# Optimization experiments

Hardware: AMD Instinct MI355X
Metric: run time of the kernel (lower is better)

Reference implementation:

```python
import jax, jax.numpy as jnp
import numpy as np

EPS = 1e-8


def setup_inputs() -> dict:
    key = jax.random.key(0)
    ks = jax.random.split(key, 11)
    N, D_OBS, D_AC, K = 2_000_000, 32, 16, 128
    H = int(1.66 * K)  # 212, matches int(1.66*k) in the torch module
    s = 0.05
    return {
        "obs": jax.random.normal(ks[0], (N, D_OBS), dtype=jnp.float32),
        "acs": jax.random.normal(ks[1], (N, D_AC), dtype=jnp.float32),
        "x": jax.random.normal(ks[2], (D_OBS,), dtype=jnp.float32),
        "w_in": jax.random.normal(ks[3], (H, K), dtype=jnp.float32) * s,
        "b_in": jax.random.normal(ks[4], (H,), dtype=jnp.float32) * s,
        "w2": jax.random.normal(ks[5], (H, H), dtype=jnp.float32) * s,
        "b2": jax.random.normal(ks[6], (H,), dtype=jnp.float32) * s,
        "w3": jax.random.normal(ks[7], (H, H), dtype=jnp.float32) * s,
        "b3": jax.random.normal(ks[8], (H,), dtype=jnp.float32) * s,
        "w_out": jax.random.normal(ks[9], (K, H), dtype=jnp.float32) * s,
        "b_out": jax.random.normal(ks[10], (K,), dtype=jnp.float32) * s,
        "k": K,
    }


def reference(obs, acs, x, w_in, b_in, w2, b2, w3, b3, w_out, b_out, k):
    # cosine distance between every obs row and the query x: [N]
    xn = x * jax.lax.rsqrt(jnp.sum(x * x) + EPS)
    obs_nrm = jax.lax.rsqrt(jnp.sum(obs * obs, axis=1) + EPS)  # [N]
    cos_sim = (obs @ xn) * obs_nrm                              # [N]
    cos_dist = 1.0 - cos_sim                                    # [N]

    # top-k smallest distances (argpartition equivalent, sorted ascending)
    neg_vals, idx = jax.lax.top_k(-cos_dist, k)                 # [k], [k]
    k_cos_dist = -neg_vals                                      # [k]
    k_actions = acs[idx]                                        # [k, D_ac]

    # tiny MLP on the k distances -> softmax weights over the k neighbors
    h = jax.nn.relu(k_cos_dist @ w_in.T + b_in)
    h = jax.nn.relu(h @ w2.T + b2)
    h = jax.nn.relu(h @ w3.T + b3)
    weights = jax.nn.softmax(h @ w_out.T + b_out)               # [k]

    # weighted sum of the k neighbor actions -> [1, D_ac]
    out = jnp.sum(weights[:, None] * k_actions, axis=0, keepdims=True)
    return out
```

## Files before the change

### kernel.cpp

```cpp
#include <hip/hip_runtime.h>
#include <math.h>

#define NBIN 4096
#define CAPC 4096
#define KSEL 128
#define HDIM 212
#define DAC  16
#define EPSF 1e-8f
#define GRID1 2048
#define TROWS 256
#define TBYTES (TROWS * 128)

__device__ __forceinline__ void gload_lds16(const void* g, void* l) {
    __builtin_amdgcn_global_load_lds(
        (const __attribute__((address_space(1))) unsigned int*)g,
        (__attribute__((address_space(3))) unsigned int*)l, 16, 0, 0);
}

__global__ void k_init(const float* __restrict__ x, float* __restrict__ xn,
                       unsigned* __restrict__ hist, unsigned* __restrict__ meta) {
    int t = threadIdx.x;
    __shared__ float rs;
    if (t < 32) {
        float v = x[t];
        float s = v * v;
        #pragma unroll
        for (int o = 16; o >= 1; o >>= 1) s += __shfl_down(s, o);
        if (t == 0) rs = rsqrtf(s + EPSF);
    }
    __syncthreads();
    if (t < 32) xn[t] = x[t] * rs;
    for (int b = t; b < NBIN; b += blockDim.x) hist[b] = 0u;
    if (t < 8) meta[t] = 0u;
}

__global__ __launch_bounds__(256) void k_cos_hist(
        const char* __restrict__ obs, const float* __restrict__ xn,
        float* __restrict__ cosb, unsigned* __restrict__ hist, int N) {
    __shared__ unsigned lhist[NBIN];
    __shared__ char tile[TBYTES];
    __shared__ float xs[32];
    for (int b = threadIdx.x; b < NBIN; b += 256) lhist[b] = 0u;
    if (threadIdx.x < 32) xs[threadIdx.x] = xn[threadIdx.x];
    __syncthreads();

    float4 X[8];
    #pragma unroll
    for (int q = 0; q < 8; q++)
        X[q] = make_float4(xs[4*q+0], xs[4*q+1], xs[4*q+2], xs[4*q+3]);

    const int t = threadIdx.x;
    const int wave = t >> 6, lane = t & 63;
    const int fullTiles = N / TROWS;

    #define D4(v, q) ((v).x*X[q].x + (v).y*X[q].y + (v).z*X[q].z + (v).w*X[q].w)
    #define N4(v)    ((v).x*(v).x + (v).y*(v).y + (v).z*(v).z + (v).w*(v).w)

    for (int tl = blockIdx.x; tl < fullTiles; tl += gridDim.x) {
        const char* gbase = obs + (size_t)tl * TBYTES;
        #pragma unroll
        for (int i = 0; i < 8; i++) {
            int dst = wave * 8192 + i * 1024;
            int o   = dst + lane * 16;
            int src = o ^ (((o >> 7) & 7) << 4);
            gload_lds16(gbase + src, tile + dst);
        }
        __syncthreads();

        const int xr = (t & 7) << 4;
        const char* rbase = tile + t * 128;
        #define RD(q) (*(const float4*)(rbase + (((q) * 16) ^ xr)))
        float4 v0 = RD(0), v1 = RD(1), v2 = RD(2), v3 = RD(3);
        float4 v4 = RD(4), v5 = RD(5), v6 = RD(6), v7 = RD(7);
        #undef RD
        float dot = (D4(v0,0) + D4(v1,1)) + (D4(v2,2) + D4(v3,3))
                  + (D4(v4,4) + D4(v5,5)) + (D4(v6,6) + D4(v7,7));
        float nrm = (N4(v0) + N4(v1)) + (N4(v2) + N4(v3))
                  + (N4(v4) + N4(v5)) + (N4(v6) + N4(v7));
        float cd = 1.0f - dot * rsqrtf(nrm + EPSF);
        cosb[tl * TROWS + t] = cd;
        unsigned u = __float_as_uint(cd);
        unsigned key = (u & 0x80000000u) ? ~u : (u | 0x80000000u);
        atomicAdd(&lhist[key >> 20], 1u);
        __syncthreads();
    }

    if (blockIdx.x == gridDim.x - 1) {
        for (int row = fullTiles * TROWS + t; row < N; row += 256) {
            const float4* rp = (const float4*)(obs + (size_t)row * 128);
            float4 v0 = rp[0], v1 = rp[1], v2 = rp[2], v3 = rp[3];
            float4 v4 = rp[4], v5 = rp[5], v6 = rp[6], v7 = rp[7];
            float dot = (D4(v0,0) + D4(v1,1)) + (D4(v2,2) + D4(v3,3))
                      + (D4(v4,4) + D4(v5,5)) + (D4(v6,6) + D4(v7,7));
            float nrm = (N4(v0) + N4(v1)) + (N4(v2) + N4(v3))
                      + (N4(v4) + N4(v5)) + (N4(v6) + N4(v7));
            float cd = 1.0f - dot * rsqrtf(nrm + EPSF);
            cosb[row] = cd;
            unsigned u = __float_as_uint(cd);
            unsigned key = (u & 0x80000000u) ? ~u : (u | 0x80000000u);
            atomicAdd(&lhist[key >> 20], 1u);
        }
    }
    #undef D4
    #undef N4

    __syncthreads();
    for (int b = threadIdx.x; b < NBIN; b += 256) {
        unsigned c = lhist[b];
        if (c) atomicAdd(&hist[b], c);
    }
}

__global__ __launch_bounds__(64) void k_scan(const unsigned* __restrict__ hist,
                                             unsigned* __restrict__ meta, int K) {
    int t = threadIdx.x;
    unsigned c[64];
    unsigned local = 0;
    #pragma unroll
    for (int q = 0; q < 64; q++) { c[q] = hist[64*t + q]; local += c[q]; }
    unsigned sc = local;
    #pragma unroll
    for (int o = 1; o < 64; o <<= 1) {
        unsigned v = __shfl_up(sc, o);
        if (t >= o) sc += v;
    }
    unsigned incl = sc, excl = sc - local;
    if (excl < (unsigned)K && (unsigned)K <= incl) {
        unsigned cum = excl;
        int B = 64*t;
        for (int q = 0; q < 64; q++) {
            cum += c[q];
            if (cum >= (unsigned)K) { B = 64*t + q; break; }
        }
        meta[1] = (B >= NBIN - 1) ? 0xFFFFFFFFu : ((unsigned)(B + 1) << 20);
    }
}

__global__ __launch_bounds__(256) void k_compact(
        const float4* __restrict__ cos4, unsigned* __restrict__ meta,
        float* __restrict__ cval, int* __restrict__ cidx, int n4, int N) {
    unsigned keyHi = meta[1];
    int g = blockIdx.x * blockDim.x + threadIdx.x;
    if (g >= n4) return;
    float4 v = cos4[g];
    float vv[4] = {v.x, v.y, v.z, v.w};
    #pragma unroll
    for (int q = 0; q < 4; q++) {
        int i = g*4 + q;
        if (i < N) {
            unsigned u = __float_as_uint(vv[q]);
            unsigned key = (u & 0x80000000u) ? ~u : (u | 0x80000000u);
            if (key < keyHi) {
                unsigned pos = atomicAdd(&meta[0], 1u);
                if (pos < CAPC) { cval[pos] = vv[q]; cidx[pos] = i; }
            }
        }
    }
}

__global__ __launch_bounds__(512) void k_final(
        const float* __restrict__ cval, const int* __restrict__ cidx,
        const unsigned* __restrict__ meta, const float* __restrict__ acs,
        const float* __restrict__ w_in, const float* __restrict__ b_in,
        const float* __restrict__ w2, const float* __restrict__ b2,
        const float* __restrict__ w3, const float* __restrict__ b3,
        const float* __restrict__ w_out, const float* __restrict__ b_out,
        float* __restrict__ out) {
    __shared__ unsigned kv[CAPC];
    __shared__ int      idv[CAPC];
    __shared__ unsigned char act[CAPC];
    __shared__ unsigned hist2[256];
    __shared__ unsigned remArr[9];
    __shared__ unsigned pivB[8];
    __shared__ unsigned selB_sh;
    __shared__ unsigned scnt;
    __shared__ unsigned skey[KSEL];
    __shared__ int      sidx[KSEL];
    __shared__ float    sval[KSEL];
    __shared__ float d[KSEL];
    __shared__ int   id2[KSEL];
    __shared__ float h1[HDIM], h2[HDIM], h3[HDIM], lg[KSEL];
    __shared__ float smax_sh, rsum_sh;

    const int t = threadIdx.x;
    int M = (int)meta[0];
    if (M > CAPC) M = CAPC;

    for (int i = t; i < M; i += 512) {
        float v = cval[i];
        unsigned u = __float_as_uint(v);
        kv[i]  = (u & 0x80000000u) ? ~u : (u | 0x80000000u);
        idv[i] = cidx[i];
        act[i] = 1;
    }
    if (t == 0) remArr[0] = KSEL - 1;
    if (t < KSEL) {
        skey[t] = 0xFFFFFFFFu; sidx[t] = 0x7FFFFFFF; sval[t] = 0.f;
        d[t] = 0.f; id2[t] = 0;
    }
    __syncthreads();

    for (int r = 0; r < 8; r++) {
        if (t < 256) hist2[t] = 0u;
        __syncthreads();
        for (int i = t; i < M; i += 512) {
            if (act[i]) {
                unsigned b = (r < 4) ? ((kv[i] >> ((3-r)*8)) & 0xFFu)
                                     : (((unsigned)idv[i] >> ((7-r)*8)) & 0xFFu);
                atomicAdd(&hist2[b], 1u);
            }
        }
        __syncthreads();
        if (t < 64) {
            unsigned s0 = hist2[4*t], s1 = hist2[4*t+1],
                     s2 = hist2[4*t+2], s3 = hist2[4*t+3];
            unsigned tot = s0 + s1 + s2 + s3;
            unsigned sc = tot;
            #pragma unroll
            for (int o = 1; o < 64; o <<= 1) {
                unsigned v2 = __shfl_up(sc, o);
                if (t >= o) sc += v2;
            }
            unsigned cb = sc - tot;
            unsigned rm = remArr[r];
            unsigned ss[4] = {s0, s1, s2, s3};
            #pragma unroll
            for (int q = 0; q < 4; q++) {
                if (cb <= rm && rm < cb + ss[q]) {
                    selB_sh = 4*t + q;
                    pivB[r] = 4*t + q;
                    remArr[r+1] = rm - cb;
                }
                cb += ss[q];
            }
        }
        __syncthreads();
        unsigned sb = selB_sh;
        for (int i = t; i < M; i += 512) {
            if (act[i]) {
                unsigned b = (r < 4) ? ((kv[i] >> ((3-r)*8)) & 0xFFu)
                                     : (((unsigned)idv[i] >> ((7-r)*8)) & 0xFFu);
                if (b != sb) act[i] = 0;
            }
        }
        __syncthreads();
    }

    unsigned kvP = (pivB[0]<<24) | (pivB[1]<<16) | (pivB[2]<<8) | pivB[3];
    unsigned idP = (pivB[4]<<24) | (pivB[5]<<16) | (pivB[6]<<8) | pivB[7];
    if (t == 0) scnt = 0u;
    __syncthreads();

    for (int i = t; i < M; i += 512) {
        unsigned k = kv[i];
        unsigned ui = (unsigned)idv[i];
        if (k < kvP || (k == kvP && ui <= idP)) {
            unsigned p = atomicAdd(&scnt, 1u);
            if (p < KSEL) {
                skey[p] = k;
                sidx[p] = idv[i];
                unsigned u = (k & 0x80000000u) ? (k & 0x7FFFFFFFu) : ~k;
                sval[p] = __uint_as_float(u);
            }
        }
    }
    __syncthreads();

    if (t < KSEL) {
        unsigned mk = skey[t], mi = (unsigned)sidx[t];
        int rank = 0;
        for (int j = 0; j < KSEL; j++) {
            unsigned jk = skey[j], ji = (unsigned)sidx[j];
            rank += (jk < mk || (jk == mk && ji < mi)) ? 1 : 0;
        }
        d[rank] = sval[t];
        id2[rank] = sidx[t];
    }
    __syncthreads();

    if (t < HDIM) {
        float s = b_in[t];
        const float* wr = &w_in[t * KSEL];
        for (int j = 0; j < KSEL; j++) s += wr[j] * d[j];
        h1[t] = s > 0.f ? s : 0.f;
    }
    __syncthreads();
    if (t < HDIM) {
        float s = b2[t];
        const float* wr = &w2[t * HDIM];
        for (int j = 0; j < HDIM; j++) s += wr[j] * h1[j];
        h2[t] = s > 0.f ? s : 0.f;
    }
    __syncthreads();
    if (t < HDIM) {
        float s = b3[t];
        const float* wr = &w3[t * HDIM];
        for (int j = 0; j < HDIM; j++) s += wr[j] * h2[j];
        h3[t] = s > 0.f ? s : 0.f;
    }
    __syncthreads();
    if (t < KSEL) {
        float s = b_out[t];
        const float* wr = &w_out[t * HDIM];
        for (int j = 0; j < HDIM; j++) s += wr[j] * h3[j];
        lg[t] = s;
    }
    __syncthreads();

    if (t < 64) {
        float a = fmaxf(lg[t], lg[t + 64]);
        #pragma unroll
        for (int o = 32; o >= 1; o >>= 1) a = fmaxf(a, __shfl_xor(a, o));
        if (t == 0) smax_sh = a;
    }
    __syncthreads();
    if (t < KSEL) lg[t] = __expf(lg[t] - smax_sh);
    __syncthreads();
    if (t < 64) {
        float s = lg[t] + lg[t + 64];
        #pragma unroll
        for (int o = 32; o >= 1; o >>= 1) s += __shfl_xor(s, o);
        if (t == 0) rsum_sh = 1.0f / s;
    }
    __syncthreads();

    if (t < DAC) {
        float s = 0.f;
        for (int j = 0; j < KSEL; j++)
            s += lg[j] * acs[(size_t)id2[j] * DAC + t];
        out[t] = s * rsum_sh;
    }
}

extern "C" void kernel_launch(void* const* d_in, const int* in_sizes, int n_in,
                              void* d_out, int out_size, void* d_ws, size_t ws_size,
                              hipStream_t stream) {
    const float* obs   = (const float*)d_in[0];
    const float* acs   = (const float*)d_in[1];
    const float* x     = (const float*)d_in[2];
    const float* w_in  = (const float*)d_in[3];
    const float* b_in  = (const float*)d_in[4];
    const float* w2    = (const float*)d_in[5];
    const float* b2    = (const float*)d_in[6];
    const float* w3    = (const float*)d_in[7];
    const float* b3    = (const float*)d_in[8];
    const float* w_out = (const float*)d_in[9];
    const float* b_out = (const float*)d_in[10];
    float* out = (float*)d_out;

    int N = in_sizes[0] / 32;

    char* ws = (char*)d_ws;
    float*    xn   = (float*)ws;
    float*    cosb = (float*)(ws + 256);
    size_t histOff = 256 + (((size_t)N * 4 + 255) / 256) * 256;
    unsigned* hist = (unsigned*)(ws + histOff);
    unsigned* meta = (unsigned*)(ws + histOff + NBIN * 4);
    float*    cval = (float*)(ws + histOff + NBIN * 4 + 256);
    int*      cidx = (int*)(ws + histOff + NBIN * 4 + 256 + CAPC * 4);

    k_init<<<1, 256, 0, stream>>>(x, xn, hist, meta);

    k_cos_hist<<<GRID1, 256, 0, stream>>>((const char*)obs, xn, cosb, hist, N);

    k_scan<<<1, 64, 0, stream>>>(hist, meta, KSEL);

    int n4 = (N + 3) / 4;
    k_compact<<<(n4 + 255) / 256, 256, 0, stream>>>((const float4*)cosb, meta,
                                                    cval, cidx, n4, N);

    k_final<<<1, 512, 0, stream>>>(cval, cidx, meta, acs, w_in, b_in,
                                   w2, b2, w3, b3, w_out, b_out, out);
}
```

Before: 136.7 us.

## Use direct nontemporal row loads in cosine pass and prefetch MLP weights

The cosine/histogram kernel drops the LDS-staged swizzled tile loads and per-tile barriers. Each thread now reads its own 128-byte row with nontemporal vector loads in a grid-stride loop. In the final MLP kernel, the otherwise idle threads (256 and above) touch the next layer's weights to warm the cache while the current layer computes, and the dot products use wider vector loads. Per-thread strided row loads may coalesce worse than the LDS staging did, and the prefetch adds extra traffic to the single-block tail.

```diff
diff --git a/kernel.cpp b/kernel.cpp
--- a/kernel.cpp
+++ b/kernel.cpp
@@ -8,14 +8,8 @@
 #define DAC  16
 #define EPSF 1e-8f
 #define GRID1 2048
-#define TROWS 256
-#define TBYTES (TROWS * 128)
-
-__device__ __forceinline__ void gload_lds16(const void* g, void* l) {
-    __builtin_amdgcn_global_load_lds(
-        (const __attribute__((address_space(1))) unsigned int*)g,
-        (__attribute__((address_space(3))) unsigned int*)l, 16, 0, 0);
-}
+
+typedef float f4v __attribute__((ext_vector_type(4)));
 
 __global__ void k_init(const float* __restrict__ x, float* __restrict__ xn,
                        unsigned* __restrict__ hist, unsigned* __restrict__ meta) {
@@ -35,74 +29,46 @@
 }
 
 __global__ __launch_bounds__(256) void k_cos_hist(
-        const char* __restrict__ obs, const float* __restrict__ xn,
+        const float* __restrict__ obs, const float* __restrict__ xn,
         float* __restrict__ cosb, unsigned* __restrict__ hist, int N) {
     __shared__ unsigned lhist[NBIN];
-    __shared__ char tile[TBYTES];
     __shared__ float xs[32];
     for (int b = threadIdx.x; b < NBIN; b += 256) lhist[b] = 0u;
     if (threadIdx.x < 32) xs[threadIdx.x] = xn[threadIdx.x];
     __syncthreads();
 
-    float4 X[8];
+    f4v X[8];
     #pragma unroll
     for (int q = 0; q < 8; q++)
-        X[q] = make_float4(xs[4*q+0], xs[4*q+1], xs[4*q+2], xs[4*q+3]);
-
-    const int t = threadIdx.x;
-    const int wave = t >> 6, lane = t & 63;
-    const int fullTiles = N / TROWS;
-
-    #define D4(v, q) ((v).x*X[q].x + (v).y*X[q].y + (v).z*X[q].z + (v).w*X[q].w)
-    #define N4(v)    ((v).x*(v).x + (v).y*(v).y + (v).z*(v).z + (v).w*(v).w)
-
-    for (int tl = blockIdx.x; tl < fullTiles; tl += gridDim.x) {
-        const char* gbase = obs + (size_t)tl * TBYTES;
-        #pragma unroll
-        for (int i = 0; i < 8; i++) {
-            int dst = wave * 8192 + i * 1024;
-            int o   = dst + lane * 16;
-            int src = o ^ (((o >> 7) & 7) << 4);
-            gload_lds16(gbase + src, tile + dst);
-        }
-        __syncthreads();
-
-        const int xr = (t & 7) << 4;
-        const char* rbase = tile + t * 128;
-        #define RD(q) (*(const float4*)(rbase + (((q) * 16) ^ xr)))
-        float4 v0 = RD(0), v1 = RD(1), v2 = RD(2), v3 = RD(3);
-        float4 v4 = RD(4), v5 = RD(5), v6 = RD(6), v7 = RD(7);
-        #undef RD
+        X[q] = (f4v){xs[4*q+0], xs[4*q+1], xs[4*q+2], xs[4*q+3]};
+
+    const int stride = gridDim.x * blockDim.x;
+    for (int row = blockIdx.x * blockDim.x + threadIdx.x; row < N; row += stride) {
+        const f4v* rp = (const f4v*)(obs + (size_t)row * 32);
+        f4v v0 = __builtin_nontemporal_load(rp + 0);
+        f4v v1 = __builtin_nontemporal_load(rp + 1);
+        f4v v2 = __builtin_nontemporal_load(rp + 2);
+        f4v v3 = __builtin_nontemporal_load(rp + 3);
+        f4v v4 = __builtin_nontemporal_load(rp + 4);
+        f4v v5 = __builtin_nontemporal_load(rp + 5);
+        f4v v6 = __builtin_nontemporal_load(rp + 6);
+        f4v v7 = __builtin_nontemporal_load(rp + 7);
+
+        #define D4(v, q) ((v)[0]*X[q][0] + (v)[1]*X[q][1] + (v)[2]*X[q][2] + (v)[3]*X[q][3])
+        #define N4(v)    ((v)[0]*(v)[0] + (v)[1]*(v)[1] + (v)[2]*(v)[2] + (v)[3]*(v)[3])
         float dot = (D4(v0,0) + D4(v1,1)) + (D4(v2,2) + D4(v3,3))
                   + (D4(v4,4) + D4(v5,5)) + (D4(v6,6) + D4(v7,7));
         float nrm = (N4(v0) + N4(v1)) + (N4(v2) + N4(v3))
                   + (N4(v4) + N4(v5)) + (N4(v6) + N4(v7));
+        #undef D4
+        #undef N4
+
         float cd = 1.0f - dot * rsqrtf(nrm + EPSF);
-        cosb[tl * TROWS + t] = cd;
+        cosb[row] = cd;
         unsigned u = __float_as_uint(cd);
         unsigned key = (u & 0x80000000u) ? ~u : (u | 0x80000000u);
         atomicAdd(&lhist[key >> 20], 1u);
-        __syncthreads();
-    }
-
-    if (blockIdx.x == gridDim.x - 1) {
-        for (int row = fullTiles * TROWS + t; row < N; row += 256) {
-            const float4* rp = (const float4*)(obs + (size_t)row * 128);
-            float4 v0 = rp[0], v1 = rp[1], v2 = rp[2], v3 = rp[3];
-            float4 v4 = rp[4], v5 = rp[5], v6 = rp[6], v7 = rp[7];
-            float dot = (D4(v0,0) + D4(v1,1)) + (D4(v2,2) + D4(v3,3))
-                      + (D4(v4,4) + D4(v5,5)) + (D4(v6,6) + D4(v7,7));
-            float nrm = (N4(v0) + N4(v1)) + (N4(v2) + N4(v3))
-                      + (N4(v4) + N4(v5)) + (N4(v6) + N4(v7));
-            float cd = 1.0f - dot * rsqrtf(nrm + EPSF);
-            cosb[row] = cd;
-            unsigned u = __float_as_uint(cd);
-            unsigned key = (u & 0x80000000u) ? ~u : (u | 0x80000000u);
-            atomicAdd(&lhist[key >> 20], 1u);
-        }
-    }
-    #undef D4
-    #undef N4
+    }
 
     __syncthreads();
     for (int b = threadIdx.x; b < NBIN; b += 256) {
@@ -280,29 +246,56 @@
 
     if (t < HDIM) {
         float s = b_in[t];
-        const float* wr = &w_in[t * KSEL];
-        for (int j = 0; j < KSEL; j++) s += wr[j] * d[j];
+        const f4v* wr = (const f4v*)&w_in[t * KSEL];
+        for (int j = 0; j < KSEL/4; j++) {
+            f4v w = wr[j];
+            s += w[0]*d[4*j] + w[1]*d[4*j+1] + w[2]*d[4*j+2] + w[3]*d[4*j+3];
+        }
         h1[t] = s > 0.f ? s : 0.f;
+    } else if (t >= 256) {
+        float acc = 0.f;
+        const f4v* p = (const f4v*)w2;
+        for (int i = t - 256; i < HDIM*HDIM/4; i += 256) acc += p[i][0];
+        asm volatile("" :: "v"(acc));
     }
     __syncthreads();
     if (t < HDIM) {
         float s = b2[t];
-        const float* wr = &w2[t * HDIM];
-        for (int j = 0; j < HDIM; j++) s += wr[j] * h1[j];
+        const float2* wr = (const float2*)&w2[t * HDIM];
+        for (int j = 0; j < HDIM/2; j++) {
+            float2 w = wr[j];
+            s += w.x*h1[2*j] + w.y*h1[2*j+1];
+        }
         h2[t] = s > 0.f ? s : 0.f;
+    } else if (t >= 256) {
+        float acc = 0.f;
+        const f4v* p = (const f4v*)w3;
+        for (int i = t - 256; i < HDIM*HDIM/4; i += 256) acc += p[i][0];
+        asm volatile("" :: "v"(acc));
     }
     __syncthreads();
     if (t < HDIM) {
         float s = b3[t];
-        const float* wr = &w3[t * HDIM];
-        for (int j = 0; j < HDIM; j++) s += wr[j] * h2[j];
+        const float2* wr = (const float2*)&w3[t * HDIM];
+        for (int j = 0; j < HDIM/2; j++) {
+            float2 w = wr[j];
+            s += w.x*h2[2*j] + w.y*h2[2*j+1];
+        }
         h3[t] = s > 0.f ? s : 0.f;
+    } else if (t >= 256) {
+        float acc = 0.f;
+        const f4v* p = (const f4v*)w_out;
+        for (int i = t - 256; i < KSEL*HDIM/4; i += 256) acc += p[i][0];
+        asm volatile("" :: "v"(acc));
     }
     __syncthreads();
     if (t < KSEL) {
         float s = b_out[t];
-        const float* wr = &w_out[t * HDIM];
-        for (int j = 0; j < HDIM; j++) s += wr[j] * h3[j];
+        const float2* wr = (const float2*)&w_out[t * HDIM];
+        for (int j = 0; j < HDIM/2; j++) {
+            float2 w = wr[j];
+            s += w.x*h3[2*j] + w.y*h3[2*j+1];
+        }
         lg[t] = s;
     }
     __syncthreads();
@@ -361,7 +354,7 @@
 
     k_init<<<1, 256, 0, stream>>>(x, xn, hist, meta);
 
-    k_cos_hist<<<GRID1, 256, 0, stream>>>((const char*)obs, xn, cosb, hist, N);
+    k_cos_hist<<<GRID1, 256, 0, stream>>>(obs, xn, cosb, hist, N);
 
     k_scan<<<1, 64, 0, stream>>>(hist, meta, KSEL);
 
```

Result: slower. 169.4 us (+24.0%).
